# Kernel tuning notes

Measured on AMD Instinct MI355X. Metric: run time of the kernel, lower is better.

## Reference

```python
import math
import jax, jax.numpy as jnp
from jax import lax
import numpy as np

THETA = 10.0      # spiking threshold
TAU_SR = 10.0     # SRM (psp) alpha-kernel time constant
TAU_REF = 1.0     # refractory alpha-kernel time constant
SCALE_REF = 2.0   # refractory scale (kernel = -scaleRef*theta*alpha)
TAU_RHO = 1.0     # surrogate-gradient width
TS = 1.0          # simulation time step


def _alpha_filter_scan(x, tau, extra_input_fn=None):
    """Causal convolution along last (time) axis with alpha kernel
    k[n] = (n*Ts/tau) * exp(1 - n*Ts/tau)  (k[0] = 0),
    implemented exactly as a 2-state linear recurrence.
    x: [N, C, T] -> out: [N, C, T]."""
    d = jnp.float32(math.exp(-TS / tau))
    c = jnp.float32(math.e * TS / tau)
    xT = jnp.moveaxis(x, -1, 0)  # [T, N, C]

    def step(carry, xt):
        p, a = carry
        a = d * (a + p)          # alpha response from inputs up to t-1
        p = d * p + xt           # pure exponential state
        return (p, a), a * c

    z = jnp.zeros_like(xT[0])
    _, out = lax.scan(step, (z, z), xT)
    return jnp.moveaxis(out, 0, -1)


def psp(x):
    return _alpha_filter_scan(x, TAU_SR)


@jax.custom_vjp
def spike_fn(v):
    # Heaviside threshold on (membrane - theta)
    return (v >= 0).astype(v.dtype)

def _spike_fwd(v):
    return spike_fn(v), v

def _spike_bwd(v, g):
    # SLAYER surrogate gradient: exponential pdf around threshold
    grad = (1.0 / TAU_RHO) * jnp.exp(-jnp.abs(v) / TAU_RHO)
    return (g * grad,)

spike_fn.defvjp(_spike_fwd, _spike_bwd)


def spike_layer(u_in):
    """Threshold-and-refract over time. u_in: [N, C, T] psp potentials.
    Refractory response = -scaleRef*theta * alpha_{tauRef}(past spikes)."""
    d = jnp.float32(math.exp(-TS / TAU_REF))
    c = jnp.float32(math.e * TS / TAU_REF)
    ref_scale = jnp.float32(-SCALE_REF * THETA)
    uT = jnp.moveaxis(u_in, -1, 0)  # [T, N, C]

    def step(carry, ut):
        p, a = carry
        a = d * (a + p)                      # refractory potential at t
        u = ut + c * a                       # membrane potential
        s = spike_fn(u - THETA)              # spikes (0/1)
        p = d * p + ref_scale * s            # inject refractory impulse
        return (p, a), s

    z = jnp.zeros_like(uT[0])
    _, s = lax.scan(step, (z, z), uT)
    return jnp.moveaxis(s, 0, -1)


def setup_inputs() -> dict:
    key = jax.random.key(0)
    k1, k2, k3 = jax.random.split(key, 3)
    N, I, H, O, T = 64, 256, 1024, 18, 500
    # Bernoulli(0.1) input spikes
    spike_input = (jax.random.uniform(k1, (N, I, T)) < 0.1).astype(jnp.float32)
    W1 = jax.random.normal(k2, (H, I), dtype=jnp.float32) * (1.0 / math.sqrt(I))
    W2 = jax.random.normal(k3, (O, H), dtype=jnp.float32) * (1.0 / math.sqrt(H))
    return {"spike_input": spike_input, "W1": W1, "W2": W2}


def reference(spike_input, W1, W2):
    # layer 1: dense (per-timestep linear) -> psp -> spike
    y1 = jnp.einsum('nit,hi->nht', spike_input, W1)
    s1 = spike_layer(psp(y1))
    # layer 2
    y2 = jnp.einsum('nht,oh->not', s1, W2)
    s2 = spike_layer(psp(y2))
    return s2
```

## Files before the change

kernel.cpp:

```cpp
#include <hip/hip_runtime.h>


#define NN 64
#define II 256
#define HH 1024
#define OO 18
#define TT 500

#define D_SR 0.9048374180359595f
#define C_SR 0.27182818284590454f
#define D_RF 0.36787944117144233f
#define C_RF 2.718281828459045f
#define THETA 10.0f
#define REFS (-20.0f)

typedef _Float16 f16;
typedef _Float16 f16x2 __attribute__((ext_vector_type(2)));
typedef _Float16 f16x8 __attribute__((ext_vector_type(8)));
typedef float f32x4 __attribute__((ext_vector_type(4)));

__device__ __forceinline__ void gl2lds16(const void* g, void* l) {
    __builtin_amdgcn_global_load_lds(
        (const __attribute__((address_space(1))) void*)g,
        (__attribute__((address_space(3))) void*)l, 16, 0, 0);
}

__launch_bounds__(256)
__global__ void prep_x(const float* __restrict__ X, f16* __restrict__ Xb) {
    __shared__ float tile[64][65];
    const int n = blockIdx.z, i0 = blockIdx.y * 64, t0 = blockIdx.x * 64;
    const int tx = threadIdx.x & 63, q = threadIdx.x >> 6;
    const float* Xn = X + (size_t)n * II * TT;
#pragma unroll 4
    for (int j = 0; j < 16; ++j) {
        int il = j * 4 + q;
        int t = t0 + tx;
        tile[il][tx] = (t < TT) ? Xn[(size_t)(i0 + il) * TT + t] : 0.f;
    }
    __syncthreads();
#pragma unroll 4
    for (int j = 0; j < 16; ++j) {
        int tl = j * 4 + q;
        int t = t0 + tl;
        if (t < TT)
            Xb[((size_t)n * TT + t) * II + i0 + tx] = (f16)tile[tx][tl];
    }
}

__launch_bounds__(256)
__global__ void prep_w1(const float* __restrict__ W1, f16* __restrict__ Wh,
                        f16* __restrict__ Wl) {
    int idx = blockIdx.x * 256 + threadIdx.x;
    float w = W1[idx];
    f16 h = (f16)w;
    f16 l = (f16)(w - (float)h);
    Wh[idx] = h;
    Wl[idx] = l;
}

__launch_bounds__(256)
__global__ void prep_w2(const float* __restrict__ W2, f16* __restrict__ Wh,
                        f16* __restrict__ Wl) {
    int idx = blockIdx.x * 256 + threadIdx.x;
    int o = idx >> 10;
    float w = (o < OO) ? W2[idx] : 0.f;
    f16 h = (f16)w;
    f16 l = (f16)(w - (float)h);
    Wh[idx] = h;
    Wl[idx] = l;
}

__launch_bounds__(256)
__global__ void gemm1_scan1(const f16* __restrict__ Xb, const f16* __restrict__ Wh,
                            const f16* __restrict__ Wl, f16* __restrict__ S1) {
    __shared__ __align__(16) char smem[128 * 132 * 4];
    float* yb = (float*)smem;

    const int tid = threadIdx.x;
    const int wave = tid >> 6, lane = tid & 63;

    const int f = blockIdx.y * 8 + blockIdx.x;
    const int x = f & 7, g = f >> 3;
    const int n = x * 8 + (g & 7);
    const int ht = g >> 3;
    const int h0g = ht * 128;

    const int rbl = wave * 32 + (lane >> 2);
    const int koff = (lane & 3) * 8;
    const f16* gBh0 = Wh + (size_t)(h0g + rbl) * II + koff;
    const f16* gBl0 = Wl + (size_t)(h0g + rbl) * II + koff;

    const int wm = wave & 1, wn = wave >> 1;
    const int fr = lane & 15, kq = lane >> 4;

    float p1 = 0.f, a1 = 0.f, p2 = 0.f, a2 = 0.f;

    for (int c = 0; c < 4; ++c) {
        const int t0 = c * 128;
        const int TCe = (TT - t0 < 128) ? (TT - t0) : 128;

        int r0 = rbl;      if (r0 > TCe - 1) r0 = TCe - 1;
        int r1 = rbl + 16; if (r1 > TCe - 1) r1 = TCe - 1;
        const f16* gA0 = Xb + ((size_t)n * TT + t0 + r0) * II + koff;
        const f16* gA1 = Xb + ((size_t)n * TT + t0 + r1) * II + koff;

        auto stage = [&](int kk2, int b) {
            f16* As_b = (f16*)(smem + b * 24576);
            f16* Bh_b = As_b + 4096;
            f16* Bl_b = As_b + 8192;
            const int ko = kk2 * 32;
            gl2lds16(gA0 + ko, As_b + wave * 1024);
            gl2lds16(gA1 + ko, As_b + wave * 1024 + 512);
            gl2lds16(gBh0 + ko, Bh_b + wave * 1024);
            gl2lds16(gBh0 + 16 * II + ko, Bh_b + wave * 1024 + 512);
            gl2lds16(gBl0 + ko, Bl_b + wave * 1024);
            gl2lds16(gBl0 + 16 * II + ko, Bl_b + wave * 1024 + 512);
        };

        stage(0, 0);

        f32x4 acc[4][4] = {};
        for (int kk = 0; kk < 8; ++kk) {
            __syncthreads();
            if (kk < 7) stage(kk + 1, (kk + 1) & 1);

            const f16* As_b = (const f16*)(smem + (kk & 1) * 24576);
            const f16* Bh_b = As_b + 4096;
            const f16* Bl_b = As_b + 8192;

            f16x8 av[4], bhv[4], blv[4];
#pragma unroll
            for (int i = 0; i < 4; ++i) {
                av[i]  = *(const f16x8*)(As_b + (wm * 64 + i * 16 + fr) * 32 + kq * 8);
                bhv[i] = *(const f16x8*)(Bh_b + (wn * 64 + i * 16 + fr) * 32 + kq * 8);
                blv[i] = *(const f16x8*)(Bl_b + (wn * 64 + i * 16 + fr) * 32 + kq * 8);
            }
#pragma unroll
            for (int i = 0; i < 4; ++i)
#pragma unroll
                for (int j = 0; j < 4; ++j) {
                    acc[i][j] = __builtin_amdgcn_mfma_f32_16x16x32_f16(av[i], bhv[j], acc[i][j], 0, 0, 0);
                    acc[i][j] = __builtin_amdgcn_mfma_f32_16x16x32_f16(av[i], blv[j], acc[i][j], 0, 0, 0);
                }
        }
        __syncthreads();

#pragma unroll
        for (int i = 0; i < 4; ++i)
#pragma unroll
            for (int j = 0; j < 4; ++j) {
                int tr = wm * 64 + i * 16 + kq * 4;
                int hc = wn * 64 + j * 16 + fr;
#pragma unroll
                for (int r = 0; r < 4; ++r)
                    yb[(tr + r) * 132 + hc] = acc[i][j][r];
            }
        __syncthreads();

        if (tid < 128) {
            float rb_[8];
#pragma unroll
            for (int j = 0; j < 8; ++j) rb_[j] = yb[j * 132 + tid];
            int t = 0;
            for (; t + 8 <= TCe; t += 8) {
#pragma unroll
                for (int j = 0; j < 8; ++j) {
                    float xv = rb_[j];
                    int tn = t + j + 8;
                    rb_[j] = (tn < TCe) ? yb[tn * 132 + tid] : 0.f;
                    a1 = D_SR * (a1 + p1);
                    p1 = D_SR * p1 + xv;
                    float ut = C_SR * a1;
                    a2 = D_RF * (a2 + p2);
                    float u = ut + C_RF * a2;
                    float s = (u >= THETA) ? 1.0f : 0.0f;
                    p2 = D_RF * p2 + REFS * s;
                    yb[(t + j) * 132 + tid] = s;
                }
            }
            int rem = TCe - t;
#pragma unroll
            for (int j = 0; j < 8; ++j) {
                if (j < rem) {
                    float xv = rb_[j];
                    a1 = D_SR * (a1 + p1);
                    p1 = D_SR * p1 + xv;
                    float ut = C_SR * a1;
                    a2 = D_RF * (a2 + p2);
                    float u = ut + C_RF * a2;
                    float s = (u >= THETA) ? 1.0f : 0.0f;
                    p2 = D_RF * p2 + REFS * s;
                    yb[(t + j) * 132 + tid] = s;
                }
            }
        }
        __syncthreads();

        const int rowq = tid >> 6;
#pragma unroll 4
        for (int pass = 0; pass < 32; ++pass) {
            int row = pass * 4 + rowq;
            if (row < TCe) {
                float v0 = yb[row * 132 + 2 * lane];
                float v1 = yb[row * 132 + 2 * lane + 1];
                f16x2 h2 = {(f16)v0, (f16)v1};
                *(f16x2*)(S1 + ((size_t)n * TT + t0 + row) * HH + h0g + 2 * lane) = h2;
            }
        }
        __syncthreads();
    }
}

__launch_bounds__(256)
__global__ void gemm2_mfma(const f16* __restrict__ S1, const f16* __restrict__ W2h,
                           const f16* __restrict__ W2l, float* __restrict__ Y2) {
    __shared__ __align__(16) f16 As[2][128 * 32];
    __shared__ __align__(16) f16 Bh[2][32 * 32];
    __shared__ __align__(16) f16 Bl[2][32 * 32];

    const int tid = threadIdx.x;
    const int wave = tid >> 6, lane = tid & 63;
    const int m0 = blockIdx.x * 128;
    const int fr = lane & 15, kq = lane >> 4;

    const f16* gA0 = S1 + (size_t)(m0 + wave * 32 + (lane >> 2)) * HH + (lane & 3) * 8;
    const f16* gA1 = gA0 + (size_t)16 * HH;
    const f16* gB = (wave < 2 ? W2h : W2l) + (size_t)((wave & 1) * 16 + (lane >> 2)) * HH + (lane & 3) * 8;

    auto stage = [&](int kk2, int b) {
        const int ko = kk2 * 32;
        gl2lds16(gA0 + ko, &As[b][wave * 1024]);
        gl2lds16(gA1 + ko, &As[b][wave * 1024 + 512]);
        gl2lds16(gB + ko, (wave < 2 ? &Bh[b][0] : &Bl[b][0]) + (wave & 1) * 512);
    };

    stage(0, 0);

    f32x4 acc[2][2] = {};
    for (int kk = 0; kk < HH / 32; ++kk) {
        __syncthreads();
        if (kk < HH / 32 - 1) stage(kk + 1, (kk + 1) & 1);
        const int b = kk & 1;

        f16x8 a[2], bh[2], bl[2];
#pragma unroll
        for (int i = 0; i < 2; ++i) {
            a[i]  = *(const f16x8*)(&As[b][(wave * 32 + i * 16 + fr) * 32 + kq * 8]);
            bh[i] = *(const f16x8*)(&Bh[b][(i * 16 + fr) * 32 + kq * 8]);
            bl[i] = *(const f16x8*)(&Bl[b][(i * 16 + fr) * 32 + kq * 8]);
        }
#pragma unroll
        for (int i = 0; i < 2; ++i)
#pragma unroll
            for (int j = 0; j < 2; ++j) {
                acc[i][j] = __builtin_amdgcn_mfma_f32_16x16x32_f16(a[i], bh[j], acc[i][j], 0, 0, 0);
                acc[i][j] = __builtin_amdgcn_mfma_f32_16x16x32_f16(a[i], bl[j], acc[i][j], 0, 0, 0);
            }
    }

#pragma unroll
    for (int i = 0; i < 2; ++i)
#pragma unroll
        for (int j = 0; j < 2; ++j) {
            int rbase = m0 + wave * 32 + i * 16 + kq * 4;
            int cc = j * 16 + fr;
            float* p = Y2 + (size_t)rbase * 32 + cc;
#pragma unroll
            for (int r = 0; r < 4; ++r)
                p[(size_t)r * 32] = acc[i][j][r];
        }
}

#define PF2 16
__launch_bounds__(64)
__global__ void scan2_k(const float* __restrict__ Y2, float* __restrict__ Out) {
    __shared__ float sb[OO * TT];
    const int n = blockIdx.x, lane = threadIdx.x;
    const float* y = Y2 + (size_t)n * TT * 32;
    const bool act = (lane < 32);

    float p1 = 0.f, a1 = 0.f, p2 = 0.f, a2 = 0.f;
    float buf[PF2];
#pragma unroll
    for (int j = 0; j < PF2; ++j) buf[j] = act ? y[j * 32 + lane] : 0.f;

    int t = 0;
    for (; t + PF2 <= TT; t += PF2) {
#pragma unroll
        for (int j = 0; j < PF2; ++j) {
            float x = buf[j];
            buf[j] = (act && t + j + PF2 < TT) ? y[(t + j + PF2) * 32 + lane] : 0.f;
            a1 = D_SR * (a1 + p1);
            p1 = D_SR * p1 + x;
            float ut = C_SR * a1;
            a2 = D_RF * (a2 + p2);
            float u = ut + C_RF * a2;
            float s = (u >= THETA) ? 1.0f : 0.0f;
            p2 = D_RF * p2 + REFS * s;
            if (lane < OO) sb[lane * TT + t + j] = s;
        }
    }
#pragma unroll
    for (int j = 0; j < PF2; ++j) {
        if (t + j < TT) {
            float x = buf[j];
            a1 = D_SR * (a1 + p1);
            p1 = D_SR * p1 + x;
            float ut = C_SR * a1;
            a2 = D_RF * (a2 + p2);
            float u = ut + C_RF * a2;
            float s = (u >= THETA) ? 1.0f : 0.0f;
            p2 = D_RF * p2 + REFS * s;
            if (lane < OO) sb[lane * TT + t + j] = s;
        }
    }
    __syncthreads();
    float* on = Out + (size_t)n * OO * TT;
    for (int e = lane; e < OO * TT; e += 64) on[e] = sb[e];
}

extern "C" void kernel_launch(void* const* d_in, const int* in_sizes, int n_in,
                              void* d_out, int out_size, void* d_ws, size_t ws_size,
                              hipStream_t stream) {
    const float* X  = (const float*)d_in[0];
    const float* W1 = (const float*)d_in[1];
    const float* W2 = (const float*)d_in[2];
    float* out = (float*)d_out;

    const size_t s_s1 = (size_t)NN * TT * HH * 2;
    const size_t s_Xb = (size_t)NN * TT * II * 2;
    const size_t s_W  = (size_t)HH * II * 2;
    const size_t s_W2 = (size_t)32 * HH * 2;

    char* w = (char*)d_ws;
    f16*   s1b = (f16*)w;  w += s_s1;
    f16*   Xb  = (f16*)w;  w += s_Xb;
    f16*   W1h = (f16*)w;  w += s_W;
    f16*   W1l = (f16*)w;  w += s_W;
    f16*   W2h = (f16*)w;  w += s_W2;
    f16*   W2l = (f16*)w;  w += s_W2;
    float* y2  = (float*)w;

    prep_x<<<dim3(8, 4, NN), 256, 0, stream>>>(X, Xb);
    prep_w1<<<(HH * II) / 256, 256, 0, stream>>>(W1, W1h, W1l);
    prep_w2<<<(32 * HH) / 256, 256, 0, stream>>>(W2, W2h, W2l);

    gemm1_scan1<<<dim3(8, NN), 256, 0, stream>>>(Xb, W1h, W1l, s1b);

    gemm2_mfma<<<(NN * TT) / 128, 256, 0, stream>>>(s1b, W2h, W2l, y2);
    scan2_k<<<NN, 64, 0, stream>>>(y2, out);
}
```

Measured before the change: 212.3 us.

## Split gemm2 K dimension across two blocks and write scan1 spikes directly

gemm2 now runs with a second grid dimension that splits the 1024-deep reduction into two halves. Each half writes its partial sums to a separate Y2 buffer, and scan2 adds the two partials as it loads them. This doubles the block count to raise occupancy on the small-N GEMM, at the cost of extra partial-sum traffic and a workspace for y2 that must be twice as large. Separately, scan1 now stores f16 spikes straight to global with a strided per-thread pattern. This removes the LDS round-trip, a barrier and the coalesced copy loop, but the global writes become uncoalesced 2-byte stores.

Result: slower. 327.1 us (+54.1%).

```diff
diff --git a/kernel.cpp b/kernel.cpp
--- a/kernel.cpp
+++ b/kernel.cpp
@@ -158,6 +158,7 @@
         __syncthreads();
 
         if (tid < 128) {
+            f16* sq = S1 + ((size_t)n * TT + t0) * HH + h0g + tid;
             float rb_[8];
 #pragma unroll
             for (int j = 0; j < 8; ++j) rb_[j] = yb[j * 132 + tid];
@@ -175,7 +176,7 @@
                     float u = ut + C_RF * a2;
                     float s = (u >= THETA) ? 1.0f : 0.0f;
                     p2 = D_RF * p2 + REFS * s;
-                    yb[(t + j) * 132 + tid] = s;
+                    sq[(size_t)(t + j) * HH] = (f16)s;
                 }
             }
             int rem = TCe - t;
@@ -190,21 +191,8 @@
                     float u = ut + C_RF * a2;
                     float s = (u >= THETA) ? 1.0f : 0.0f;
                     p2 = D_RF * p2 + REFS * s;
-                    yb[(t + j) * 132 + tid] = s;
+                    sq[(size_t)(t + j) * HH] = (f16)s;
                 }
-            }
-        }
-        __syncthreads();
-
-        const int rowq = tid >> 6;
-#pragma unroll 4
-        for (int pass = 0; pass < 32; ++pass) {
-            int row = pass * 4 + rowq;
-            if (row < TCe) {
-                float v0 = yb[row * 132 + 2 * lane];
-                float v1 = yb[row * 132 + 2 * lane + 1];
-                f16x2 h2 = {(f16)v0, (f16)v1};
-                *(f16x2*)(S1 + ((size_t)n * TT + t0 + row) * HH + h0g + 2 * lane) = h2;
             }
         }
         __syncthreads();
@@ -221,11 +209,13 @@
     const int tid = threadIdx.x;
     const int wave = tid >> 6, lane = tid & 63;
     const int m0 = blockIdx.x * 128;
+    const int kh = blockIdx.y;
+    const int kbase = kh * 512;
     const int fr = lane & 15, kq = lane >> 4;
 
-    const f16* gA0 = S1 + (size_t)(m0 + wave * 32 + (lane >> 2)) * HH + (lane & 3) * 8;
+    const f16* gA0 = S1 + (size_t)(m0 + wave * 32 + (lane >> 2)) * HH + kbase + (lane & 3) * 8;
     const f16* gA1 = gA0 + (size_t)16 * HH;
-    const f16* gB = (wave < 2 ? W2h : W2l) + (size_t)((wave & 1) * 16 + (lane >> 2)) * HH + (lane & 3) * 8;
+    const f16* gB = (wave < 2 ? W2h : W2l) + (size_t)((wave & 1) * 16 + (lane >> 2)) * HH + kbase + (lane & 3) * 8;
 
     auto stage = [&](int kk2, int b) {
         const int ko = kk2 * 32;
@@ -237,9 +227,9 @@
     stage(0, 0);
 
     f32x4 acc[2][2] = {};
-    for (int kk = 0; kk < HH / 32; ++kk) {
+    for (int kk = 0; kk < 16; ++kk) {
         __syncthreads();
-        if (kk < HH / 32 - 1) stage(kk + 1, (kk + 1) & 1);
+        if (kk < 15) stage(kk + 1, (kk + 1) & 1);
         const int b = kk & 1;
 
         f16x8 a[2], bh[2], bl[2];
@@ -258,13 +248,14 @@
             }
     }
 
+    float* Yh = Y2 + (size_t)kh * NN * TT * 32;
 #pragma unroll
     for (int i = 0; i < 2; ++i)
 #pragma unroll
         for (int j = 0; j < 2; ++j) {
             int rbase = m0 + wave * 32 + i * 16 + kq * 4;
             int cc = j * 16 + fr;
-            float* p = Y2 + (size_t)rbase * 32 + cc;
+            float* p = Yh + (size_t)rbase * 32 + cc;
 #pragma unroll
             for (int r = 0; r < 4; ++r)
                 p[(size_t)r * 32] = acc[i][j][r];
@@ -276,20 +267,23 @@
 __global__ void scan2_k(const float* __restrict__ Y2, float* __restrict__ Out) {
     __shared__ float sb[OO * TT];
     const int n = blockIdx.x, lane = threadIdx.x;
-    const float* y = Y2 + (size_t)n * TT * 32;
+    const float* ya = Y2 + (size_t)n * TT * 32;
+    const float* yb2 = Y2 + (size_t)NN * TT * 32 + (size_t)n * TT * 32;
     const bool act = (lane < 32);
 
     float p1 = 0.f, a1 = 0.f, p2 = 0.f, a2 = 0.f;
     float buf[PF2];
 #pragma unroll
-    for (int j = 0; j < PF2; ++j) buf[j] = act ? y[j * 32 + lane] : 0.f;
+    for (int j = 0; j < PF2; ++j)
+        buf[j] = act ? (ya[j * 32 + lane] + yb2[j * 32 + lane]) : 0.f;
 
     int t = 0;
     for (; t + PF2 <= TT; t += PF2) {
 #pragma unroll
         for (int j = 0; j < PF2; ++j) {
             float x = buf[j];
-            buf[j] = (act && t + j + PF2 < TT) ? y[(t + j + PF2) * 32 + lane] : 0.f;
+            int tn = t + j + PF2;
+            buf[j] = (act && tn < TT) ? (ya[tn * 32 + lane] + yb2[tn * 32 + lane]) : 0.f;
             a1 = D_SR * (a1 + p1);
             p1 = D_SR * p1 + x;
             float ut = C_SR * a1;
@@ -347,6 +341,6 @@
 
     gemm1_scan1<<<dim3(8, NN), 256, 0, stream>>>(Xb, W1h, W1l, s1b);
 
-    gemm2_mfma<<<(NN * TT) / 128, 256, 0, stream>>>(s1b, W2h, W2l, y2);
+    gemm2_mfma<<<dim3((NN * TT) / 128, 2), 256, 0, stream>>>(s1b, W2h, W2l, y2);
     scan2_k<<<NN, 64, 0, stream>>>(y2, out);
 }
```
